# Kernel tuning notes

Hardware: AMD Instinct MI355X
Metric: run time of the kernel (lower is better)

## Reference

```python
import jax, jax.numpy as jnp
import numpy as np

N_HEAD, D_MODEL, D_HEAD = 16, 1024, 64
BSZ, SEQLEN = 2, 2048
ROPE_BASE = 10000.0


def _rope_tables(seqlen, d_head, base=ROPE_BASE):
    # freqs_cis = exp(i * t * theta_j), theta_j = base^(-2j/d_head)
    inv_freq = 1.0 / (base ** (np.arange(0, d_head, 2, dtype=np.float32) / d_head))
    t = np.arange(seqlen, dtype=np.float32)
    ang = np.outer(t, inv_freq)  # [S, d_head//2]
    return jnp.asarray(np.cos(ang)), jnp.asarray(np.sin(ang))


def setup_inputs() -> dict:
    key = jax.random.key(0)
    ks = jax.random.split(key, 5)
    x = jax.random.normal(ks[0], (BSZ, SEQLEN, D_MODEL), dtype=jnp.float32)
    freqs_cos, freqs_sin = _rope_tables(SEQLEN, D_HEAD)
    scale = 0.02
    # weights stored as (in, out) so projection is x @ w
    wq = jax.random.normal(ks[1], (D_MODEL, N_HEAD * D_HEAD), dtype=jnp.float32) * scale
    wk = jax.random.normal(ks[2], (D_MODEL, N_HEAD * D_HEAD), dtype=jnp.float32) * scale
    wv = jax.random.normal(ks[3], (D_MODEL, N_HEAD * D_HEAD), dtype=jnp.float32) * scale
    wo = jax.random.normal(ks[4], (N_HEAD * D_HEAD, D_MODEL), dtype=jnp.float32) * scale
    return {"x": x, "freqs_cos": freqs_cos, "freqs_sin": freqs_sin,
            "wq": wq, "wk": wk, "wv": wv, "wo": wo}


def _apply_rope(t, cos, sin):
    # t: [B, S, H, Dh]; complex pairs are consecutive elements (x0 + i*x1)
    B, S, H, Dh = t.shape
    tf = t.astype(jnp.float32).reshape(B, S, H, Dh // 2, 2)
    t0, t1 = tf[..., 0], tf[..., 1]
    c = cos[None, :, None, :]  # [1, S, 1, Dh//2]
    s = sin[None, :, None, :]
    o0 = t0 * c - t1 * s
    o1 = t0 * s + t1 * c
    return jnp.stack([o0, o1], axis=-1).reshape(B, S, H, Dh).astype(t.dtype)


def reference(x, freqs_cos, freqs_sin, wq, wk, wv, wo):
    B, S, _ = x.shape
    H, Dh = N_HEAD, D_HEAD
    q = jnp.einsum('bsd,de->bse', x, wq).reshape(B, S, H, Dh)
    k = jnp.einsum('bsd,de->bse', x, wk).reshape(B, S, H, Dh)
    v = jnp.einsum('bsd,de->bse', x, wv).reshape(B, S, H, Dh)
    q = _apply_rope(q, freqs_cos, freqs_sin)
    k = _apply_rope(k, freqs_cos, freqs_sin)
    # [B, H, S, Dh]
    q = q.transpose(0, 2, 1, 3)
    k = k.transpose(0, 2, 1, 3)
    v = v.transpose(0, 2, 1, 3)
    scores = jnp.einsum('bhqd,bhkd->bhqk', q, k) / jnp.sqrt(jnp.float32(Dh))
    probs = jax.nn.softmax(scores.astype(jnp.float32), axis=-1).astype(q.dtype)
    out = jnp.einsum('bhqk,bhkd->bhqd', probs, v)  # [B, H, S, Dh]
    out = out.transpose(0, 2, 1, 3).reshape(B, S, H * Dh)
    return jnp.einsum('bse,ed->bsd', out, wo)
```

## Files before the change

kernel.cpp:

```cpp
#include <hip/hip_runtime.h>
#include <math.h>

#define BSZ 2
#define SEQ 2048
#define NH 16
#define DH 64
#define DM 1024
#define HD 1024

typedef _Float16 h16;
typedef _Float16 half8 __attribute__((ext_vector_type(8)));
typedef _Float16 half4 __attribute__((ext_vector_type(4)));
typedef float f32x4 __attribute__((ext_vector_type(4)));

__device__ __forceinline__ f32x4 mfma16(half8 a, half8 b, f32x4 c) {
    return __builtin_amdgcn_mfma_f32_16x16x32_f16(a, b, c, 0, 0, 0);
}

__device__ __forceinline__ void async_copy16(h16* lds, const h16* g) {
    __builtin_amdgcn_global_load_lds(
        (const __attribute__((address_space(1))) unsigned int*)g,
        (__attribute__((address_space(3))) unsigned int*)lds, 16, 0, 0);
}

#define SWZ(cb, r) ((((cb) ^ ((r) & 7)) * 8))

#define PSA(r, c) ((r) * 128 + (((((c) >> 3) ^ ((r) & 15)) << 3) | ((c) & 7)))
#define OBA(r, c) ((r) * 64 + ((((c) >> 2) ^ ((r) & 15)) << 2))

#define EXP2(x) __builtin_amdgcn_exp2f(x)

__global__ __launch_bounds__(256) void prep_kernel(
    const float* __restrict__ x, const float* __restrict__ wq,
    const float* __restrict__ wk, const float* __restrict__ wv,
    const float* __restrict__ wo,
    h16* __restrict__ x16, h16* __restrict__ wt)
{
    const int z = blockIdx.z;
    const int t = threadIdx.x;
    if (z == 4) {
        int flat = blockIdx.y * 16 + blockIdx.x;
#pragma unroll
        for (int i = 0; i < 8; ++i) {
            int idx = flat * 16384 + i * 2048 + t * 8;
            float4 a = *(const float4*)&x[idx];
            float4 b = *(const float4*)&x[idx + 4];
            half8 o;
            o[0] = (h16)a.x; o[1] = (h16)a.y; o[2] = (h16)a.z; o[3] = (h16)a.w;
            o[4] = (h16)b.x; o[5] = (h16)b.y; o[6] = (h16)b.z; o[7] = (h16)b.w;
            *(half8*)&x16[idx] = o;
        }
        return;
    }
    const float* w = (z == 0) ? wq : (z == 1) ? wk : (z == 2) ? wv : wo;
    h16* ot = wt + (size_t)z * DM * DM;
    __shared__ float tile[64][68];
    const int k0 = blockIdx.y * 64, n0 = blockIdx.x * 64;
    const int r = t >> 2, c4 = (t & 3) * 16;
#pragma unroll
    for (int i = 0; i < 16; i += 4) {
        float4 v = *(const float4*)&w[(size_t)(k0 + r) * DM + n0 + c4 + i];
        tile[r][c4 + i + 0] = v.x; tile[r][c4 + i + 1] = v.y;
        tile[r][c4 + i + 2] = v.z; tile[r][c4 + i + 3] = v.w;
    }
    __syncthreads();
#pragma unroll
    for (int g = 0; g < 2; ++g) {
        half8 hh;
#pragma unroll
        for (int j = 0; j < 8; ++j)
            hh[j] = (h16)tile[c4 + g * 8 + j][r];
        *(half8*)&ot[(size_t)(n0 + r) * DM + k0 + c4 + g * 8] = hh;
    }
}

__global__ __launch_bounds__(512, 4) void qkv_kernel(
    const h16* __restrict__ x16, const h16* __restrict__ wt,
    const float* __restrict__ fcos, const float* __restrict__ fsin,
    h16* __restrict__ Q16, h16* __restrict__ K16, h16* __restrict__ VT16)
{
    const int z = blockIdx.z;
    const h16* __restrict__ bw = wt + (size_t)z * DM * DM;

    __shared__ h16 smem[17408];
    h16* As = smem;
    h16* Bs = smem + 8192;
    h16* Vt = smem;

    const int m0 = blockIdx.y * 128;
    const int n0 = blockIdx.x * 128;
    const int t  = threadIdx.x;
    const int w  = t >> 6, ln = t & 63;
    const int L  = ln & 15, U = ln >> 4;
    const int wm = (w & 3) * 32;
    const int wn = (w >> 2) * 64;

    const int sr  = ln >> 3;
    const int scb = (ln & 7) ^ sr;

    f32x4 acc[2][4];
#pragma unroll
    for (int i = 0; i < 2; ++i)
#pragma unroll
        for (int j = 0; j < 4; ++j) acc[i][j] = (f32x4)0.0f;

    for (int k0 = 0; k0 < DM; k0 += 64) {
        __syncthreads();
#pragma unroll
        for (int c = 0; c < 2; ++c) {
            int rb = w * 16 + c * 8;
            async_copy16(&As[rb * 64], &x16[(size_t)(m0 + rb + sr) * DM + k0 + scb * 8]);
            async_copy16(&Bs[rb * 64], &bw [(size_t)(n0 + rb + sr) * DM + k0 + scb * 8]);
        }
        __syncthreads();

#pragma unroll
        for (int ks = 0; ks < 2; ++ks) {
            half8 af[2], bf[4];
#pragma unroll
            for (int mt = 0; mt < 2; ++mt)
                af[mt] = *(const half8*)&As[(wm + mt * 16 + L) * 64 + SWZ(ks * 4 + U, L)];
#pragma unroll
            for (int nt = 0; nt < 4; ++nt)
                bf[nt] = *(const half8*)&Bs[(wn + nt * 16 + L) * 64 + SWZ(ks * 4 + U, L)];
#pragma unroll
            for (int mt = 0; mt < 2; ++mt)
#pragma unroll
                for (int nt = 0; nt < 4; ++nt)
                    acc[mt][nt] = mfma16(bf[nt], af[mt], acc[mt][nt]);
        }
    }

    const int b = m0 >> 11;
    const int sbase = m0 & 2047;

    if (z < 2) {
        const float sc = (z == 0) ? 0.125f * 1.44269504088896f : 1.0f;
#pragma unroll
        for (int mt = 0; mt < 2; ++mt) {
            int s = sbase + wm + mt * 16 + L;
            const float* ct = &fcos[s * 32];
            const float* st = &fsin[s * 32];
#pragma unroll
            for (int nt = 0; nt < 4; ++nt) {
                int nl = n0 + wn + nt * 16 + U * 4;
                int d = nl & 63, h = nl >> 6;
                int pd = d >> 1;
                float cv0 = ct[pd], sv0 = st[pd];
                float cv1 = ct[pd + 1], sv1 = st[pd + 1];
                float v0 = acc[mt][nt][0], v1 = acc[mt][nt][1];
                float v2 = acc[mt][nt][2], v3 = acc[mt][nt][3];
                float o0 = (v0 * cv0 - v1 * sv0) * sc;
                float o1 = (v0 * sv0 + v1 * cv0) * sc;
                float o2 = (v2 * cv1 - v3 * sv1) * sc;
                float o3 = (v2 * sv1 + v3 * cv1) * sc;
                size_t addr = ((size_t)(b * NH + h) * SEQ + s) * DH + d;
                half4 kk;
                kk[0] = (h16)o0; kk[1] = (h16)o1; kk[2] = (h16)o2; kk[3] = (h16)o3;
                if (z == 0) *(half4*)&Q16[addr] = kk;
                else        *(half4*)&K16[addr] = kk;
            }
        }
    } else {
        __syncthreads();
#pragma unroll
        for (int mt = 0; mt < 2; ++mt)
#pragma unroll
            for (int nt = 0; nt < 4; ++nt)
#pragma unroll
                for (int r = 0; r < 4; ++r) {
                    int nloc = wn + nt * 16 + U * 4 + r;
                    int sloc = wm + mt * 16 + L;
                    Vt[nloc * 136 + sloc] = (h16)acc[mt][nt][r];
                }
        __syncthreads();
#pragma unroll
        for (int i = 0; i < 4; ++i) {
            int c = i * 512 + t;
            int dl = c >> 4;
            int s8 = (c & 15) * 8;
            half8 vv = *(const half8*)&Vt[dl * 136 + s8];
            int n = n0 + dl;
            int d = n & 63, h = n >> 6;
            *(half8*)&VT16[((size_t)(b * NH + h) * DH + d) * SEQ + sbase + s8] = vv;
        }
    }
}

__global__ __launch_bounds__(512, 4) void attn_kernel(
    const h16* __restrict__ Q16, const h16* __restrict__ K16,
    const h16* __restrict__ VT16, h16* __restrict__ A16)
{
    __shared__ h16 smem[40960];
    h16* Ks  = smem;
    h16* VTs = smem + 8192;
    h16* Ps  = smem + 24576;
    float* lbuf = (float*)smem;
    float* Obuf = (float*)Ps;

    const int t = threadIdx.x, w = t >> 6, ln = t & 63;
    const int L = ln & 15, U = ln >> 4;
    const int pair = w >> 1, half = w & 1;
    const int qw = pair * 32, kh = half * 64;
    const int q0 = blockIdx.x * 128;
    const int bh = blockIdx.y;
    const size_t base = (size_t)bh * SEQ * DH;

    half8 qf[2][2];
#pragma unroll
    for (int qb = 0; qb < 2; ++qb)
#pragma unroll
        for (int ks = 0; ks < 2; ++ks)
            qf[qb][ks] = *(const half8*)&Q16[base + (size_t)(q0 + qw + qb * 16 + L) * DH + ks * 32 + U * 8];

    half8 one8;
#pragma unroll
    for (int i = 0; i < 8; ++i) one8[i] = (h16)1.0f;

    f32x4 O[4][2];
    f32x4 lsum[2];
#pragma unroll
    for (int dt = 0; dt < 4; ++dt)
#pragma unroll
        for (int qb = 0; qb < 2; ++qb) O[dt][qb] = (f32x4)0.0f;
    lsum[0] = (f32x4)0.0f;
    lsum[1] = (f32x4)0.0f;

    const int sr  = ln >> 3;
    const int scb = (ln & 7) ^ sr;

#pragma unroll
    for (int c = 0; c < 2; ++c) {
        int rv = (w * 2 + c) * 4;
        int c16 = (ln & 15) ^ ((rv + U) & 15);
        async_copy16(&VTs[rv * 128], &VT16[base + (size_t)(rv + U) * SEQ + c16 * 8]);
    }
#pragma unroll
    for (int c = 0; c < 2; ++c) {
        int rbk = c * 64 + w * 8;
        async_copy16(&Ks[rbk * 64], &K16[base + (size_t)(rbk + sr) * DH + scb * 8]);
    }

    for (int j0 = 0; j0 < SEQ; j0 += 128) {
        const int buf = (j0 >> 7) & 1;
        h16* VTcur = VTs + buf * 8192;

        asm volatile("s_waitcnt vmcnt(0)" ::: "memory");
        __builtin_amdgcn_s_barrier();
        __builtin_amdgcn_sched_barrier(0);

        if (j0 + 128 < SEQ) {
            h16* VTnxt = VTs + (buf ^ 1) * 8192;
#pragma unroll
            for (int c = 0; c < 2; ++c) {
                int rv = (w * 2 + c) * 4;
                int c16 = (ln & 15) ^ ((rv + U) & 15);
                async_copy16(&VTnxt[rv * 128],
                             &VT16[base + (size_t)(rv + U) * SEQ + (j0 + 128) + c16 * 8]);
            }
        }

        f32x4 S[4][2];
        __builtin_amdgcn_s_setprio(1);
#pragma unroll
        for (int nt = 0; nt < 4; ++nt) {
            S[nt][0] = (f32x4)0.0f;
            S[nt][1] = (f32x4)0.0f;
#pragma unroll
            for (int ks = 0; ks < 2; ++ks) {
                half8 kf = *(const half8*)&Ks[(kh + nt * 16 + L) * 64 + SWZ(ks * 4 + U, L)];
                S[nt][0] = mfma16(kf, qf[0][ks], S[nt][0]);
                S[nt][1] = mfma16(kf, qf[1][ks], S[nt][1]);
            }
        }
        __builtin_amdgcn_s_setprio(0);

        asm volatile("s_waitcnt lgkmcnt(0)" ::: "memory");
        __builtin_amdgcn_sched_barrier(0);
        __builtin_amdgcn_s_barrier();

        if (j0 + 128 < SEQ) {
#pragma unroll
            for (int c = 0; c < 2; ++c) {
                int rbk = c * 64 + w * 8;
                async_copy16(&Ks[rbk * 64],
                             &K16[base + (size_t)(j0 + 128 + rbk + sr) * DH + scb * 8]);
            }
        }

#pragma unroll
        for (int qb = 0; qb < 2; ++qb) {
            int prow = qw + qb * 16 + L;
#pragma unroll
            for (int nt = 0; nt < 4; ++nt) {
                half4 pq;
                pq[0] = (h16)EXP2(S[nt][qb][0]);
                pq[1] = (h16)EXP2(S[nt][qb][1]);
                pq[2] = (h16)EXP2(S[nt][qb][2]);
                pq[3] = (h16)EXP2(S[nt][qb][3]);
                *(half4*)&Ps[PSA(prow, kh + nt * 16 + U * 4)] = pq;
            }
        }

        half8 pf[2][2];
#pragma unroll
        for (int qb = 0; qb < 2; ++qb)
#pragma unroll
            for (int ks2 = 0; ks2 < 2; ++ks2)
                pf[qb][ks2] = *(const half8*)&Ps[PSA(qw + qb * 16 + L, kh + ks2 * 32 + U * 8)];

        __builtin_amdgcn_s_setprio(1);
#pragma unroll
        for (int dt = 0; dt < 4; ++dt)
#pragma unroll
            for (int ks2 = 0; ks2 < 2; ++ks2) {
                half8 vf = *(const half8*)&VTcur[(dt * 16 + L) * 128 + ((half * 8 + ks2 * 4 + U) ^ L) * 8];
                O[dt][0] = mfma16(vf, pf[0][ks2], O[dt][0]);
                O[dt][1] = mfma16(vf, pf[1][ks2], O[dt][1]);
            }
#pragma unroll
        for (int ks2 = 0; ks2 < 2; ++ks2) {
            lsum[0] = mfma16(one8, pf[0][ks2], lsum[0]);
            lsum[1] = mfma16(one8, pf[1][ks2], lsum[1]);
        }
        __builtin_amdgcn_s_setprio(0);
    }

    if (U == 0) {
        lbuf[w * 32 + L]      = lsum[0][0];
        lbuf[w * 32 + 16 + L] = lsum[1][0];
    }
    __syncthreads();
    const int pw = w ^ 1;
    float l_tot[2];
    l_tot[0] = lsum[0][0] + lbuf[pw * 32 + L];
    l_tot[1] = lsum[1][0] + lbuf[pw * 32 + 16 + L];

    if (half) {
#pragma unroll
        for (int qb = 0; qb < 2; ++qb)
#pragma unroll
            for (int dt = 0; dt < 4; ++dt)
                *(f32x4*)&Obuf[OBA(qw + qb * 16 + L, dt * 16 + U * 4)] = O[dt][qb];
    }
    __syncthreads();
    if (!half) {
        const int b = bh >> 4, hh = bh & 15;
#pragma unroll
        for (int qb = 0; qb < 2; ++qb) {
            float inv = 1.0f / l_tot[qb];
            int s = q0 + qw + qb * 16 + L;
#pragma unroll
            for (int dt = 0; dt < 4; ++dt) {
                f32x4 op = *(const f32x4*)&Obuf[OBA(qw + qb * 16 + L, dt * 16 + U * 4)];
                half4 o4;
#pragma unroll
                for (int r = 0; r < 4; ++r)
                    o4[r] = (h16)((O[dt][qb][r] + op[r]) * inv);
                *(half4*)&A16[(size_t)(b * SEQ + s) * HD + hh * DH + dt * 16 + U * 4] = o4;
            }
        }
    }
}

__global__ __launch_bounds__(512, 4) void oproj_kernel(
    const h16* __restrict__ A16, const h16* __restrict__ bw,
    float* __restrict__ out)
{
    __shared__ h16 As[128 * 64];
    __shared__ h16 Bs[64 * 64];

    const int m0 = blockIdx.y * 128;
    const int n0 = blockIdx.x * 64;
    const int t  = threadIdx.x;
    const int w  = t >> 6, ln = t & 63;
    const int L  = ln & 15, U = ln >> 4;

    const int sr  = ln >> 3;
    const int scb = (ln & 7) ^ sr;

    f32x4 acc[4];
#pragma unroll
    for (int j = 0; j < 4; ++j) acc[j] = (f32x4)0.0f;

    for (int k0 = 0; k0 < DM; k0 += 64) {
        __syncthreads();
#pragma unroll
        for (int c = 0; c < 2; ++c) {
            int rb = w * 16 + c * 8;
            async_copy16(&As[rb * 64], &A16[(size_t)(m0 + rb + sr) * DM + k0 + scb * 8]);
        }
        {
            int rb = w * 8;
            async_copy16(&Bs[rb * 64], &bw[(size_t)(n0 + rb + sr) * DM + k0 + scb * 8]);
        }
        __syncthreads();

#pragma unroll
        for (int ks = 0; ks < 2; ++ks) {
            half8 af, bf[4];
            af = *(const half8*)&As[(w * 16 + L) * 64 + SWZ(ks * 4 + U, L)];
#pragma unroll
            for (int nt = 0; nt < 4; ++nt)
                bf[nt] = *(const half8*)&Bs[(nt * 16 + L) * 64 + SWZ(ks * 4 + U, L)];
#pragma unroll
            for (int nt = 0; nt < 4; ++nt)
                acc[nt] = mfma16(af, bf[nt], acc[nt]);
        }
    }

#pragma unroll
    for (int nt = 0; nt < 4; ++nt)
#pragma unroll
        for (int r = 0; r < 4; ++r) {
            int row = m0 + w * 16 + U * 4 + r;
            int col = n0 + nt * 16 + L;
            out[(size_t)row * DM + col] = acc[nt][r];
        }
}

extern "C" void kernel_launch(void* const* d_in, const int* in_sizes, int n_in,
                              void* d_out, int out_size, void* d_ws, size_t ws_size,
                              hipStream_t stream)
{
    const float* x    = (const float*)d_in[0];
    const float* fcos = (const float*)d_in[1];
    const float* fsin = (const float*)d_in[2];
    const float* wq   = (const float*)d_in[3];
    const float* wk   = (const float*)d_in[4];
    const float* wv   = (const float*)d_in[5];
    const float* wo   = (const float*)d_in[6];
    float* out = (float*)d_out;

    const size_t M4 = (size_t)4 * 1024 * 1024;
    h16* x16  = (h16*)d_ws;
    h16* wt   = x16 + M4;
    h16* Q16  = wt + M4;
    h16* K16  = Q16 + M4;
    h16* VT16 = K16 + M4;
    h16* A16  = VT16 + M4;

    prep_kernel<<<dim3(16, 16, 5), 256, 0, stream>>>(x, wq, wk, wv, wo, x16, wt);
    qkv_kernel<<<dim3(8, 32, 3), 512, 0, stream>>>(x16, wt, fcos, fsin,
                                                   Q16, K16, VT16);
    attn_kernel<<<dim3(16, 32), 512, 0, stream>>>(Q16, K16, VT16, A16);
    oproj_kernel<<<dim3(16, 32), 512, 0, stream>>>(A16, wt + 3 * (size_t)DM * DM, out);
}
```

Measured before the change: 187.5 us.

## Double-buffer LDS loads in QKV and O-proj GEMMs and remap block order for XCDs

The QKV and output-projection GEMMs now use two LDS buffers: the next k-tile is fetched with async global-to-LDS copies while MFMAs run on the current tile, with a single waitcnt and barrier per iteration in place of two syncthreads. Block indices in all three kernels are permuted so consecutive blocks spread across XCDs and neighbouring tiles share L2. s_setprio is raised around the MFMA section. This doubles LDS use in the QKV kernel to 64KB, which can lower occupancy.

```diff
diff --git a/kernel.cpp b/kernel.cpp
--- a/kernel.cpp
+++ b/kernel.cpp
@@ -79,16 +79,17 @@
     const float* __restrict__ fcos, const float* __restrict__ fsin,
     h16* __restrict__ Q16, h16* __restrict__ K16, h16* __restrict__ VT16)
 {
-    const int z = blockIdx.z;
+    const int id  = (blockIdx.z * 32 + blockIdx.y) * 8 + blockIdx.x;
+    const int swz = (id & 7) * 96 + (id >> 3);
+    const int z   = swz >> 8;
+    const int m0  = ((swz >> 3) & 31) * 128;
+    const int n0  = (swz & 7) * 128;
+
     const h16* __restrict__ bw = wt + (size_t)z * DM * DM;
 
-    __shared__ h16 smem[17408];
-    h16* As = smem;
-    h16* Bs = smem + 8192;
+    __shared__ h16 smem[32768];
     h16* Vt = smem;
 
-    const int m0 = blockIdx.y * 128;
-    const int n0 = blockIdx.x * 128;
     const int t  = threadIdx.x;
     const int w  = t >> 6, ln = t & 63;
     const int L  = ln & 15, U = ln >> 4;
@@ -104,16 +105,35 @@
 #pragma unroll
         for (int j = 0; j < 4; ++j) acc[i][j] = (f32x4)0.0f;
 
+#pragma unroll
+    for (int c = 0; c < 2; ++c) {
+        int rb = w * 16 + c * 8;
+        async_copy16(&smem[rb * 64],        &x16[(size_t)(m0 + rb + sr) * DM + scb * 8]);
+        async_copy16(&smem[8192 + rb * 64], &bw [(size_t)(n0 + rb + sr) * DM + scb * 8]);
+    }
+
     for (int k0 = 0; k0 < DM; k0 += 64) {
-        __syncthreads();
-#pragma unroll
-        for (int c = 0; c < 2; ++c) {
-            int rb = w * 16 + c * 8;
-            async_copy16(&As[rb * 64], &x16[(size_t)(m0 + rb + sr) * DM + k0 + scb * 8]);
-            async_copy16(&Bs[rb * 64], &bw [(size_t)(n0 + rb + sr) * DM + k0 + scb * 8]);
-        }
-        __syncthreads();
-
+        const int buf = (k0 >> 6) & 1;
+        h16* As = smem + buf * 16384;
+        h16* Bs = As + 8192;
+
+        asm volatile("s_waitcnt vmcnt(0)" ::: "memory");
+        __builtin_amdgcn_s_barrier();
+        __builtin_amdgcn_sched_barrier(0);
+
+        if (k0 + 64 < DM) {
+            h16* An = smem + (buf ^ 1) * 16384;
+#pragma unroll
+            for (int c = 0; c < 2; ++c) {
+                int rb = w * 16 + c * 8;
+                async_copy16(&An[rb * 64],
+                             &x16[(size_t)(m0 + rb + sr) * DM + k0 + 64 + scb * 8]);
+                async_copy16(&An[8192 + rb * 64],
+                             &bw [(size_t)(n0 + rb + sr) * DM + k0 + 64 + scb * 8]);
+            }
+        }
+
+        __builtin_amdgcn_s_setprio(1);
 #pragma unroll
         for (int ks = 0; ks < 2; ++ks) {
             half8 af[2], bf[4];
@@ -129,6 +149,7 @@
                 for (int nt = 0; nt < 4; ++nt)
                     acc[mt][nt] = mfma16(bf[nt], af[mt], acc[mt][nt]);
         }
+        __builtin_amdgcn_s_setprio(0);
     }
 
     const int b = m0 >> 11;
@@ -202,8 +223,11 @@
     const int L = ln & 15, U = ln >> 4;
     const int pair = w >> 1, half = w & 1;
     const int qw = pair * 32, kh = half * 64;
-    const int q0 = blockIdx.x * 128;
-    const int bh = blockIdx.y;
+
+    const int id  = blockIdx.y * 16 + blockIdx.x;
+    const int swz = (id & 7) * 64 + (id >> 3);
+    const int q0  = (swz & 15) * 128;
+    const int bh  = swz >> 4;
     const size_t base = (size_t)bh * SEQ * DH;
 
     half8 qf[2][2];
@@ -367,11 +391,13 @@
     const h16* __restrict__ A16, const h16* __restrict__ bw,
     float* __restrict__ out)
 {
-    __shared__ h16 As[128 * 64];
-    __shared__ h16 Bs[64 * 64];
-
-    const int m0 = blockIdx.y * 128;
-    const int n0 = blockIdx.x * 64;
+    __shared__ h16 smem[24576];
+
+    const int id  = blockIdx.y * 16 + blockIdx.x;
+    const int swz = (id & 7) * 64 + (id >> 3);
+    const int n0  = (swz & 15) * 64;
+    const int m0  = (swz >> 4) * 128;
+
     const int t  = threadIdx.x;
     const int w  = t >> 6, ln = t & 63;
     const int L  = ln & 15, U = ln >> 4;
@@ -383,19 +409,35 @@
 #pragma unroll
     for (int j = 0; j < 4; ++j) acc[j] = (f32x4)0.0f;
 
+#pragma unroll
+    for (int c = 0; c < 2; ++c) {
+        int rb = w * 16 + c * 8;
+        async_copy16(&smem[rb * 64], &A16[(size_t)(m0 + rb + sr) * DM + scb * 8]);
+    }
+    async_copy16(&smem[8192 + (w * 8) * 64], &bw[(size_t)(n0 + w * 8 + sr) * DM + scb * 8]);
+
     for (int k0 = 0; k0 < DM; k0 += 64) {
-        __syncthreads();
-#pragma unroll
-        for (int c = 0; c < 2; ++c) {
-            int rb = w * 16 + c * 8;
-            async_copy16(&As[rb * 64], &A16[(size_t)(m0 + rb + sr) * DM + k0 + scb * 8]);
-        }
-        {
-            int rb = w * 8;
-            async_copy16(&Bs[rb * 64], &bw[(size_t)(n0 + rb + sr) * DM + k0 + scb * 8]);
-        }
-        __syncthreads();
-
+        const int buf = (k0 >> 6) & 1;
+        h16* As = smem + buf * 12288;
+        h16* Bs = As + 8192;
+
+        asm volatile("s_waitcnt vmcnt(0)" ::: "memory");
+        __builtin_amdgcn_s_barrier();
+        __builtin_amdgcn_sched_barrier(0);
+
+        if (k0 + 64 < DM) {
+            h16* An = smem + (buf ^ 1) * 12288;
+#pragma unroll
+            for (int c = 0; c < 2; ++c) {
+                int rb = w * 16 + c * 8;
+                async_copy16(&An[rb * 64],
+                             &A16[(size_t)(m0 + rb + sr) * DM + k0 + 64 + scb * 8]);
+            }
+            async_copy16(&An[8192 + (w * 8) * 64],
+                         &bw[(size_t)(n0 + w * 8 + sr) * DM + k0 + 64 + scb * 8]);
+        }
+
+        __builtin_amdgcn_s_setprio(1);
 #pragma unroll
         for (int ks = 0; ks < 2; ++ks) {
             half8 af, bf[4];
@@ -407,6 +449,7 @@
             for (int nt = 0; nt < 4; ++nt)
                 acc[nt] = mfma16(af, bf[nt], acc[nt]);
         }
+        __builtin_amdgcn_s_setprio(0);
     }
 
 #pragma unroll
```

Result: faster. 179.3 us (-4.4%).
